# Kernel tuning notes

Measured on AMD Instinct MI355X. Metric: run time of the kernel, lower is better.

Reference implementation:

```python
import jax, jax.numpy as jnp
import numpy as np

ACTION_NS = [3, 3, 2, 4, 24]        # forward_back, left_right, jump, sneak_sprint, attack_...
RANGE_STARTS = [6, 8, 10, 11, 14]   # action_ranges starts (indices 0..5 are commit + camera ops)
N_ACTIONS = 37
LOGIT_DIM = 36
MIN_DELTA = 0.5 / 2**3
MAX_STEP = 20
MAX_CAMSTEP = 6
B, NUM_INPUT, HIDDEN = 32768, 1024, 2048
D_IN = NUM_INPUT + 4 + LOGIT_DIM


def setup_inputs():
    key = jax.random.key(0)
    ks = jax.random.split(key, 12)
    inp = {
        "fc_input": jax.random.normal(ks[0], (B, NUM_INPUT), jnp.float32),
        "camera": jax.random.normal(ks[1], (B, 2), jnp.float32),
        "rand_u": jax.random.uniform(ks[2], (B,), jnp.float32),
        "W1": (jax.random.normal(ks[3], (D_IN, HIDDEN), jnp.float32) / np.sqrt(D_IN)).astype(jnp.float32),
        "b1": jnp.zeros((HIDDEN,), jnp.float32),
        "W2": (jax.random.normal(ks[4], (HIDDEN, N_ACTIONS), jnp.float32) / np.sqrt(HIDDEN)).astype(jnp.float32),
        "b2": jnp.zeros((N_ACTIONS,), jnp.float32),
    }
    names = ["act_fb", "act_lr", "act_jp", "act_ss", "act_atk"]
    for i, (nm, n) in enumerate(zip(names, ACTION_NS)):
        inp[nm] = jax.random.randint(ks[5 + i], (B,), 0, n, jnp.int32)
    return inp


def _discretize_scan(camera, acts):
    # Faithful jax version of the 20-step no_grad target/input construction loop.
    nB = camera.shape[0]
    cam0, cam1 = camera[:, 0], camera[:, 1]

    def step(carry, _):
        ac, delta, rdac, dch, cam_steps, committed, norm = carry
        oh = [jax.nn.one_hot(r, n, dtype=jnp.float32) for r, n in zip(rdac, ACTION_NS)]
        inp_vec = jnp.concatenate([ac] + oh + [delta[:, None], dch.astype(jnp.float32)[:, None]], axis=1)  # [B,40]
        norm = norm + (~committed).astype(jnp.float32)
        commit = ((jnp.abs(cam0) < 1e-5) & (jnp.abs(cam1) < 1e-5)) | (cam_steps >= MAX_CAMSTEP)
        for r, a in zip(rdac, acts):
            commit = commit & (r == a)
        dac = jnp.zeros((nB,), jnp.int32)
        modified = commit
        new_rdac = []
        for r, a, rs in zip(rdac, acts, RANGE_STARTS):
            disc = (~modified) & (r != a)
            dac = jnp.where(disc & (a == 0), r - 1 + rs, jnp.where(disc, a - 1 + rs, dac))
            new_rdac.append(jnp.where(disc, a, r))
            modified = modified | disc
        d2 = delta * 2.0
        # NOTE: original torch code compares cam[:,1] against ac[:,0]; bug preserved.
        dmask = (~modified) & (~dch) & ((jnp.abs(cam0 - ac[:, 0]) > d2) | (jnp.abs(cam1 - ac[:, 0]) > d2))
        dac = jnp.where(dmask, 5, dac)
        delta = jnp.where(dmask, jnp.clip(d2, -0.5, 0.5), delta)
        modified = modified | dmask
        sx = jnp.where(cam0 < ac[:, 0], -1.0, 1.0)
        sy = jnp.where(cam1 < ac[:, 1], -1.0, 1.0)
        quad = jnp.where(sx < 0, jnp.where(sy < 0, 1, 3), jnp.where(sy < 0, 2, 4)).astype(jnp.int32)
        dac = jnp.where(~modified, quad, dac)
        move = jnp.stack([sx, sy], axis=1) * delta[:, None]
        ac = jnp.where((~modified)[:, None], ac + move, ac)
        delta = jnp.where(~modified, delta * 0.5, delta)
        dch = dch | (~modified)
        cam_steps = cam_steps + (~modified).astype(jnp.int32)
        committed = committed | commit
        return (ac, delta, tuple(new_rdac), dch, cam_steps, committed, norm), (inp_vec, dac)

    init = (jnp.zeros((nB, 2), jnp.float32),
            jnp.full((nB,), MIN_DELTA, jnp.float32),
            tuple(jnp.zeros((nB,), jnp.int32) for _ in ACTION_NS),
            jnp.zeros((nB,), bool),
            jnp.zeros((nB,), jnp.int32),
            jnp.zeros((nB,), bool),
            jnp.zeros((nB,), jnp.float32))
    carry, (all_inputs, all_dacs) = jax.lax.scan(step, init, None, length=MAX_STEP)
    return all_inputs, all_dacs, carry[-1]  # [T,B,40], [T,B], norm [B]


def reference(fc_input, camera, rand_u, W1, b1, W2, b2, act_fb, act_lr, act_jp, act_ss, act_atk):
    acts = (act_fb, act_lr, act_jp, act_ss, act_atk)
    all_inputs, all_dacs, norm = _discretize_scan(camera, acts)
    rand_sam = jnp.minimum((rand_u * norm).astype(jnp.int32), MAX_STEP - 1)  # sample an uncommitted step
    idx = jnp.arange(fc_input.shape[0])
    sel = jax.lax.stop_gradient(all_inputs[rand_sam, idx])  # [B,40]
    tgt = jax.lax.stop_gradient(all_dacs[rand_sam, idx])    # [B]
    x = jnp.concatenate([fc_input, sel], axis=1)
    h = x @ W1 + b1
    h = h * jax.nn.sigmoid(h)  # swish
    logits = h @ W2 + b2
    logp = jax.nn.log_softmax(logits, axis=-1)
    loss = -jnp.take_along_axis(logp, tgt[:, None], axis=1)[:, 0]  # per-sample CE (reduction='none')
    return loss
```

## Files before the change

kernel.cpp:

```cpp
#include <hip/hip_runtime.h>
#include <hip/hip_bf16.h>
#include <stdint.h>

#define B_ROWS 32768
#define NUM_IN 1024
#define D_PAD2 1088
#define HID    2048
#define NPAD   64

typedef __attribute__((ext_vector_type(8))) short bf16x8;
typedef __attribute__((ext_vector_type(4))) float f32x4;
typedef unsigned short ushort_t;

__device__ __forceinline__ unsigned short f2bf(float f){
  union { float f; uint32_t u; } x; x.f = f;
  uint32_t u = x.u;
  return (unsigned short)((u + 0x7FFFu + ((u >> 16) & 1u)) >> 16);
}

__device__ __forceinline__ void gload16(const void* g, void* l){
  __builtin_amdgcn_global_load_lds((const __attribute__((address_space(1))) void*)g,
                                   (__attribute__((address_space(3))) void*)l, 16, 0, 0);
}

__device__ __forceinline__ int disc_step(
    float cam0, float cam1, const int a[5],
    float& ac0, float& ac1, float& delta,
    int r[5], bool& dch, int& cam_steps, bool& committed, float& norm)
{
  const int RS[5] = {6, 8, 10, 11, 14};
  norm += committed ? 0.0f : 1.0f;
  bool commit = ((fabsf(cam0) < 1e-5f) && (fabsf(cam1) < 1e-5f)) || (cam_steps >= 6);
  #pragma unroll
  for (int i = 0; i < 5; ++i) commit = commit && (r[i] == a[i]);
  int dac = 0;
  bool modified = commit;
  #pragma unroll
  for (int i = 0; i < 5; ++i){
    bool disc = (!modified) && (r[i] != a[i]);
    if (disc){
      dac = (a[i] == 0) ? (r[i] - 1 + RS[i]) : (a[i] - 1 + RS[i]);
      r[i] = a[i];
      modified = true;
    }
  }
  float d2 = delta * 2.0f;
  bool dmask = (!modified) && (!dch) &&
               ((fabsf(cam0 - ac0) > d2) || (fabsf(cam1 - ac0) > d2));
  if (dmask){ dac = 5; delta = fminf(d2, 0.5f); modified = true; }
  if (!modified){
    float sx = (cam0 < ac0) ? -1.0f : 1.0f;
    float sy = (cam1 < ac1) ? -1.0f : 1.0f;
    dac = (sx < 0.0f) ? ((sy < 0.0f) ? 1 : 3) : ((sy < 0.0f) ? 2 : 4);
    ac0 += sx * delta; ac1 += sy * delta;
    delta *= 0.5f;
    dch = true;
    cam_steps += 1;
  }
  committed = committed || commit;
  return dac;
}

__global__ void k_prep(const float* __restrict__ fc, const float* __restrict__ W1,
                       const float* __restrict__ W2,
                       const float* __restrict__ camera, const float* __restrict__ rand_u,
                       const int* __restrict__ afb, const int* __restrict__ alr,
                       const int* __restrict__ ajp, const int* __restrict__ ass,
                       const int* __restrict__ aat,
                       unsigned short* __restrict__ xb, unsigned short* __restrict__ w1p,
                       unsigned short* __restrict__ w2t, int* __restrict__ tgt)
{
  __shared__ float lt[64][65];
  const int b = blockIdx.x;
  const int tid = threadIdx.x;
  if (b < 16384){
    int gid = b * 256 + tid;
    int row = gid >> 7;
    int c   = gid & 127;
    const float4* p = (const float4*)(fc + (size_t)row * NUM_IN + c * 8);
    float4 f0 = p[0], f1 = p[1];
    uint4 pk;
    pk.x = (uint32_t)f2bf(f0.x) | ((uint32_t)f2bf(f0.y) << 16);
    pk.y = (uint32_t)f2bf(f0.z) | ((uint32_t)f2bf(f0.w) << 16);
    pk.z = (uint32_t)f2bf(f1.x) | ((uint32_t)f2bf(f1.y) << 16);
    pk.w = (uint32_t)f2bf(f1.z) | ((uint32_t)f2bf(f1.w) << 16);
    *(uint4*)(xb + (size_t)row * D_PAD2 + c * 8) = pk;
    return;
  }
  if (b < 16928){
    const int bi = b - 16384;
    const int kt = bi % 17, nt = bi / 17;
    const int k0 = kt * 64, n0 = nt * 64;
    const int cgrp = nt >> 2, wn = nt & 3;
    const int c = tid & 63, rq = tid >> 6;
    #pragma unroll
    for (int rr = 0; rr < 16; ++rr){
      const int r = rr * 4 + rq;
      const int k = k0 + r;
      lt[r][c] = (k < 1064) ? W1[(size_t)k * HID + n0 + c] : 0.0f;
    }
    __syncthreads();
    #pragma unroll
    for (int s = 0; s < 2; ++s){
      const int idx = s * 256 + tid;
      const int ln = idx & 63, q = idx >> 6;
      const int lr2 = ln & 15, lg2 = ln >> 4;
      const int np = (q >> 2) * 32 + ((q >> 1) & 1) * 16 + lr2;
      const int kx = (q & 1) * 32 + lg2 * 8;
      uint4 pk;
      uint32_t w[4];
      #pragma unroll
      for (int e = 0; e < 4; ++e){
        unsigned short lo = f2bf(lt[kx + 2*e][np]);
        unsigned short hi = f2bf(lt[kx + 2*e + 1][np]);
        w[e] = (uint32_t)lo | ((uint32_t)hi << 16);
      }
      pk.x = w[0]; pk.y = w[1]; pk.z = w[2]; pk.w = w[3];
      *(uint4*)(w1p + (((size_t)cgrp*17 + kt) << 14) + (wn << 12) + q*512 + ln*8) = pk;
    }
    return;
  }
  if (b < 17440){
    int idx = (b - 16928) * 256 + tid;
    int n = idx >> 11;
    int k = idx & (HID - 1);
    float v = (n < 37) ? W2[(size_t)k * 37 + n] : 0.0f;
    w2t[idx] = f2bf(v);
    return;
  }
  int row = (b - 17440) * 256 + tid;
  float cam0 = camera[2*row], cam1 = camera[2*row + 1];
  int a[5] = { afb[row], alr[row], ajp[row], ass[row], aat[row] };

  float ac0 = 0.f, ac1 = 0.f, delta = 0.0625f, norm = 0.f;
  int r[5] = {0,0,0,0,0};
  bool dch = false, committed = false; int cam_steps = 0;
  for (int t = 0; t < 20; ++t)
    disc_step(cam0, cam1, a, ac0, ac1, delta, r, dch, cam_steps, committed, norm);

  int rs = (int)(rand_u[row] * norm);
  if (rs > 19) rs = 19;
  if (rs < 0) rs = 0;

  ac0 = 0.f; ac1 = 0.f; delta = 0.0625f; norm = 0.f;
  r[0]=r[1]=r[2]=r[3]=r[4]=0; dch = false; committed = false; cam_steps = 0;
  for (int t = 0; t < rs; ++t)
    disc_step(cam0, cam1, a, ac0, ac1, delta, r, dch, cam_steps, committed, norm);

  float vec[40];
  #pragma unroll
  for (int j = 0; j < 40; ++j) vec[j] = 0.0f;
  vec[0] = ac0; vec[1] = ac1;
  const int offs[5] = {2, 5, 8, 10, 14};
  #pragma unroll
  for (int i = 0; i < 5; ++i) vec[offs[i] + r[i]] = 1.0f;
  vec[38] = delta; vec[39] = dch ? 1.0f : 0.0f;

  int dac = disc_step(cam0, cam1, a, ac0, ac1, delta, r, dch, cam_steps, committed, norm);
  tgt[row] = dac;

  unsigned short* o = xb + (size_t)row * D_PAD2 + NUM_IN;
  #pragma unroll
  for (int j = 0; j < 40; ++j) o[j] = f2bf(vec[j]);
  #pragma unroll
  for (int j = 40; j < 64; ++j) o[j] = 0;
}


#define STAGE(REG, KT, HALF) do { \
    const ushort_t* s0_ = xb + (size_t)(brow + (HALF)*128 + srow) * D_PAD2 + ((KT) << 6) + scol; \
    gload16(s0_, lds + (REG) + (HALF)*8192 + t*8); \
    gload16(s0_ + (size_t)64 * D_PAD2, lds + (REG) + (HALF)*8192 + 4096 + t*8); \
  } while(0)

#define LDA_T(BO, MH) do { \
    _Pragma("unroll") for (int mi_ = 0; mi_ < 4; ++mi_) \
    _Pragma("unroll") for (int kk_ = 0; kk_ < 2; ++kk_) \
      aR[mi_][kk_] = *(const bf16x8*)(aBk[kk_] + (BO) + (((MH)*64 + mi_*16)*128)); \
  } while(0)

#define GLBH(BANK, KT, NH) do { \
    const ushort_t* bp_ = w1p + (((size_t)cgrp*17 + (KT)) << 14) + (wn << 12) + ((NH)*4)*512 + lane*8; \
    _Pragma("unroll") for (int ni_ = 0; ni_ < 2; ++ni_) \
    _Pragma("unroll") for (int kk_ = 0; kk_ < 2; ++kk_) \
      BANK[ni_][kk_] = *(const bf16x8*)(bp_ + (ni_*2 + kk_)*512); \
  } while(0)

#define MMA(MH, NH, BH) do { \
    __builtin_amdgcn_s_setprio(1); \
    _Pragma("unroll") for (int mi_ = 0; mi_ < 4; ++mi_) \
    _Pragma("unroll") for (int ni_ = 0; ni_ < 2; ++ni_) \
    _Pragma("unroll") for (int kk_ = 0; kk_ < 2; ++kk_) \
      acc[(MH)*4+mi_][(NH)*2+ni_] = __builtin_amdgcn_mfma_f32_16x16x32_bf16( \
          aR[mi_][kk_], BH[ni_][kk_], acc[(MH)*4+mi_][(NH)*2+ni_], 0, 0, 0); \
    __builtin_amdgcn_s_setprio(0); \
  } while(0)

#define BAR() __builtin_amdgcn_s_barrier()
#define WAIT_VM4() asm volatile("s_waitcnt vmcnt(4)" ::: "memory")
#define WAIT_VM0() asm volatile("s_waitcnt vmcnt(0)" ::: "memory")

__global__ __launch_bounds__(512, 2) void k_gemm1(const ushort_t* __restrict__ xb,
                                                  const ushort_t* __restrict__ w1p,
                                                  const ushort_t* __restrict__ w2t,
                                                  const float* __restrict__ b1,
                                                  float* __restrict__ pbuf)
{
  __shared__ ushort_t lds[65536];
  const int t = threadIdx.x;
  const int lane = t & 63;
  const int wid = t >> 6, wm = wid >> 2, wn = wid & 3;
  const int lr = lane & 15, lg = lane >> 4;

  const int bid = blockIdx.x;
  const int swz = (bid & 7) * 128 + (bid >> 3);
  const int brow = (swz >> 3) << 8;
  const int bcol = (swz & 7) << 8;
  const int cgrp = bcol >> 8;

  const int srow = t >> 3;
  const int scol = ((t & 7) ^ (srow & 7)) << 3;

  const int axor = lr & 7;
  const char* aBk[2];
  aBk[0] = (const char*)lds + (wm*128 + lr)*128 + (((0*4+lg)^axor) << 4);
  aBk[1] = (const char*)lds + (wm*128 + lr)*128 + (((1*4+lg)^axor) << 4);

  f32x4 acc[8][4] = {};
  bf16x8 aR[4][2];
  bf16x8 bH0[2][2], bH1[2][2];

  STAGE(0, 0, 0);  STAGE(0, 0, 1);
  GLBH(bH0, 0, 0); GLBH(bH1, 0, 1);
  STAGE(16384, 1, 0);  STAGE(16384, 1, 1);
  WAIT_VM4();
  BAR();

  #pragma unroll
  for (int tt = 0; tt < 17; ++tt){
    const int cbuf = (tt % 3) * 32768;
    const int sbo  = ((tt + 2) % 3) * 16384;
    const int st   = (tt + 2 <= 16) ? tt + 2 : 16;
    const int nk   = (tt + 1 <= 16) ? tt + 1 : 16;

    LDA_T(cbuf, 0);
    MMA(0, 0, bH0);
    MMA(0, 1, bH1);
    LDA_T(cbuf, 1);
    MMA(1, 0, bH0);
    GLBH(bH0, nk, 0);
    MMA(1, 1, bH1);
    GLBH(bH1, nk, 1);
    __builtin_amdgcn_sched_barrier(0);
    STAGE(sbo, st, 0);
    STAGE(sbo, st, 1);
    WAIT_VM4();
    BAR();
  }

  bf16x8 w2fA[4][4];
  #pragma unroll
  for (int ks = 0; ks < 4; ++ks)
    #pragma unroll
    for (int ni = 0; ni < 4; ++ni)
      w2fA[ks][ni] = *(const bf16x8*)(w2t + (size_t)(ni*16 + lr) * HID + bcol + ks*32 + lg*8);

  WAIT_VM0();
  BAR();

  float b1v[4];
  #pragma unroll
  for (int ni = 0; ni < 4; ++ni) b1v[ni] = b1[bcol + wn*64 + ni*16 + lr];

  #pragma unroll
  for (int mi = 0; mi < 8; ++mi){
    #pragma unroll
    for (int ni = 0; ni < 4; ++ni){
      const int col = wn*64 + ni*16 + lr;
      #pragma unroll
      for (int i2 = 0; i2 < 4; ++i2){
        const int row = wm*128 + mi*16 + lg*4 + i2;
        float v = acc[mi][ni][i2] + b1v[ni];
        float s = v / (1.0f + __expf(-v));
        const int chunk = (col >> 3) ^ (row & 7);
        lds[row*256 + chunk*8 + (col & 7)] = f2bf(s);
      }
    }
  }
  __syncthreads();

  bf16x8 w2fB[4][4];
  #pragma unroll
  for (int ks = 0; ks < 4; ++ks)
    #pragma unroll
    for (int ni = 0; ni < 4; ++ni)
      w2fB[ks][ni] = *(const bf16x8*)(w2t + (size_t)(ni*16 + lr) * HID + bcol + (ks+4)*32 + lg*8);

  const int rb = wid * 32;
  f32x4 acc2[2][4] = {};
  #pragma unroll
  for (int ks = 0; ks < 8; ++ks){
    bf16x8 a2[2];
    #pragma unroll
    for (int m = 0; m < 2; ++m){
      const int row = rb + m*16 + lr;
      a2[m] = *(const bf16x8*)(lds + row*256 + (((ks*4+lg) ^ (lr & 7)) << 3));
    }
    #pragma unroll
    for (int m = 0; m < 2; ++m)
      #pragma unroll
      for (int ni = 0; ni < 4; ++ni)
        acc2[m][ni] = __builtin_amdgcn_mfma_f32_16x16x32_bf16(
            a2[m], (ks < 4) ? w2fA[ks & 3][ni] : w2fB[ks & 3][ni], acc2[m][ni], 0, 0, 0);
  }

  const int cb = cgrp;
  #pragma unroll
  for (int m = 0; m < 2; ++m)
    #pragma unroll
    for (int ni = 0; ni < 4; ++ni)
      #pragma unroll
      for (int i2 = 0; i2 < 4; ++i2){
        const int r = brow + rb + m*16 + lg*4 + i2;
        pbuf[((size_t)cb << 21) + ((size_t)r << 6) + ni*16 + lr] = acc2[m][ni][i2];
      }
}

__global__ __launch_bounds__(256) void k_red(const float* __restrict__ pbuf,
                                             const float* __restrict__ b2,
                                             const int* __restrict__ tgt,
                                             float* __restrict__ loss)
{
  const int lane = threadIdx.x & 63, w = threadIdx.x >> 6;
  const int row0 = blockIdx.x * 128 + w * 32;
  const float bias = (lane < 37) ? b2[lane] : 0.0f;
  for (int i = 0; i < 32; ++i){
    const int r = row0 + i;
    float s = 0.0f;
    #pragma unroll
    for (int cb = 0; cb < 8; ++cb)
      s += pbuf[((size_t)cb << 21) + ((size_t)r << 6) + lane];
    float x = (lane < 37) ? (s + bias) : -1e30f;
    float m = x;
    #pragma unroll
    for (int off = 1; off < 64; off <<= 1) m = fmaxf(m, __shfl_xor(m, off, 64));
    float e = __expf(x - m);
    float se = e;
    #pragma unroll
    for (int off = 1; off < 64; off <<= 1) se += __shfl_xor(se, off, 64);
    const int tg = tgt[r];
    const float pick = __shfl(x, tg, 64);
    if (lane == 0) loss[r] = m + __logf(se) - pick;
  }
}

extern "C" void kernel_launch(void* const* d_in, const int* in_sizes, int n_in,
                              void* d_out, int out_size, void* d_ws, size_t ws_size,
                              hipStream_t stream)
{
  (void)in_sizes; (void)n_in; (void)out_size; (void)ws_size;
  const float* fc  = (const float*)d_in[0];
  const float* cam = (const float*)d_in[1];
  const float* ru  = (const float*)d_in[2];
  const float* W1  = (const float*)d_in[3];
  const float* b1  = (const float*)d_in[4];
  const float* W2  = (const float*)d_in[5];
  const float* b2  = (const float*)d_in[6];
  const int* afb = (const int*)d_in[7];
  const int* alr = (const int*)d_in[8];
  const int* ajp = (const int*)d_in[9];
  const int* ass = (const int*)d_in[10];
  const int* aat = (const int*)d_in[11];
  float* loss = (float*)d_out;

  char* ws = (char*)d_ws;
  unsigned short* xb  = (unsigned short*)(ws);
  unsigned short* w1p = (unsigned short*)(ws + 71303168);
  unsigned short* w2t = (unsigned short*)(ws + 75759616);
  int*            tgt = (int*)           (ws + 76021760);
  float*          pbuf= (float*)         (ws + 76152832);

  k_prep<<<17568, 256, 0, stream>>>(fc, W1, W2, cam, ru, afb, alr, ajp, ass, aat,
                                    xb, w1p, w2t, tgt);
  k_gemm1<<<(B_ROWS/256) * (HID/256), 512, 0, stream>>>(xb, w1p, w2t, b1, pbuf);
  k_red  <<<B_ROWS / 128, 256, 0, stream>>>(pbuf, b2, tgt, loss);
}
```

Measured before the change: 275.3 us.

## Fuse fp32-to-bf16 conversion of fc_input into GEMM1 A-tile staging

Drops the separate prep pass that converted fc_input to a padded bf16 buffer. GEMM1 now reads fp32 fc_input directly, converts it in registers and writes swizzled bf16 into LDS, taking only the 64-column discretization tail from a small side buffer. This avoids writing and re-reading a roughly 70 MB intermediate. In exchange, each GEMM block reads fp32 A data (twice the bytes), and each of the 8 column blocks rereads it. The async global-to-LDS loads become register round trips, which adds VGPR pressure and LDS-write stalls inside the MFMA loop.

```diff
diff --git a/kernel.cpp b/kernel.cpp
--- a/kernel.cpp
+++ b/kernel.cpp
@@ -4,7 +4,6 @@
 
 #define B_ROWS 32768
 #define NUM_IN 1024
-#define D_PAD2 1088
 #define HID    2048
 #define NPAD   64
 
@@ -16,11 +15,6 @@
   union { float f; uint32_t u; } x; x.f = f;
   uint32_t u = x.u;
   return (unsigned short)((u + 0x7FFFu + ((u >> 16) & 1u)) >> 16);
-}
-
-__device__ __forceinline__ void gload16(const void* g, void* l){
-  __builtin_amdgcn_global_load_lds((const __attribute__((address_space(1))) void*)g,
-                                   (__attribute__((address_space(3))) void*)l, 16, 0, 0);
 }
 
 __device__ __forceinline__ int disc_step(
@@ -61,35 +55,19 @@
   return dac;
 }
 
-__global__ void k_prep(const float* __restrict__ fc, const float* __restrict__ W1,
-                       const float* __restrict__ W2,
+__global__ void k_prep(const float* __restrict__ W1, const float* __restrict__ W2,
                        const float* __restrict__ camera, const float* __restrict__ rand_u,
                        const int* __restrict__ afb, const int* __restrict__ alr,
                        const int* __restrict__ ajp, const int* __restrict__ ass,
                        const int* __restrict__ aat,
-                       unsigned short* __restrict__ xb, unsigned short* __restrict__ w1p,
+                       unsigned short* __restrict__ xtail, unsigned short* __restrict__ w1p,
                        unsigned short* __restrict__ w2t, int* __restrict__ tgt)
 {
   __shared__ float lt[64][65];
   const int b = blockIdx.x;
   const int tid = threadIdx.x;
-  if (b < 16384){
-    int gid = b * 256 + tid;
-    int row = gid >> 7;
-    int c   = gid & 127;
-    const float4* p = (const float4*)(fc + (size_t)row * NUM_IN + c * 8);
-    float4 f0 = p[0], f1 = p[1];
-    uint4 pk;
-    pk.x = (uint32_t)f2bf(f0.x) | ((uint32_t)f2bf(f0.y) << 16);
-    pk.y = (uint32_t)f2bf(f0.z) | ((uint32_t)f2bf(f0.w) << 16);
-    pk.z = (uint32_t)f2bf(f1.x) | ((uint32_t)f2bf(f1.y) << 16);
-    pk.w = (uint32_t)f2bf(f1.z) | ((uint32_t)f2bf(f1.w) << 16);
-    *(uint4*)(xb + (size_t)row * D_PAD2 + c * 8) = pk;
-    return;
-  }
-  if (b < 16928){
-    const int bi = b - 16384;
-    const int kt = bi % 17, nt = bi / 17;
+  if (b < 544){
+    const int kt = b % 17, nt = b / 17;
     const int k0 = kt * 64, n0 = nt * 64;
     const int cgrp = nt >> 2, wn = nt & 3;
     const int c = tid & 63, rq = tid >> 6;
@@ -120,15 +98,15 @@
     }
     return;
   }
-  if (b < 17440){
-    int idx = (b - 16928) * 256 + tid;
+  if (b < 1056){
+    int idx = (b - 544) * 256 + tid;
     int n = idx >> 11;
     int k = idx & (HID - 1);
     float v = (n < 37) ? W2[(size_t)k * 37 + n] : 0.0f;
     w2t[idx] = f2bf(v);
     return;
   }
-  int row = (b - 17440) * 256 + tid;
+  int row = (b - 1056) * 256 + tid;
   float cam0 = camera[2*row], cam1 = camera[2*row + 1];
   int a[5] = { afb[row], alr[row], ajp[row], ass[row], aat[row] };
 
@@ -159,19 +137,13 @@
   int dac = disc_step(cam0, cam1, a, ac0, ac1, delta, r, dch, cam_steps, committed, norm);
   tgt[row] = dac;
 
-  unsigned short* o = xb + (size_t)row * D_PAD2 + NUM_IN;
+  unsigned short* o = xtail + (size_t)row * 64;
   #pragma unroll
   for (int j = 0; j < 40; ++j) o[j] = f2bf(vec[j]);
   #pragma unroll
   for (int j = 40; j < 64; ++j) o[j] = 0;
 }
 
-
-#define STAGE(REG, KT, HALF) do { \
-    const ushort_t* s0_ = xb + (size_t)(brow + (HALF)*128 + srow) * D_PAD2 + ((KT) << 6) + scol; \
-    gload16(s0_, lds + (REG) + (HALF)*8192 + t*8); \
-    gload16(s0_ + (size_t)64 * D_PAD2, lds + (REG) + (HALF)*8192 + 4096 + t*8); \
-  } while(0)
 
 #define LDA_T(BO, MH) do { \
     _Pragma("unroll") for (int mi_ = 0; mi_ < 4; ++mi_) \
@@ -196,11 +168,38 @@
     __builtin_amdgcn_s_setprio(0); \
   } while(0)
 
+#define LOADH(DST, KT, H) do { \
+    const float4* fp_ = (const float4*)(fc + (size_t)(brow + s_r) * NUM_IN + ((KT) << 6) + s_h*32 + (H)*16); \
+    _Pragma("unroll") for (int j_ = 0; j_ < 4; ++j_) DST[j_] = fp_[j_]; \
+  } while(0)
+
+#define WRITEH(SRC, SBO, H) do { \
+    _Pragma("unroll") for (int cc_ = 0; cc_ < 2; ++cc_){ \
+      float4 u_ = SRC[2*cc_], v_ = SRC[2*cc_ + 1]; \
+      uint4 pk_; \
+      pk_.x = (uint32_t)f2bf(u_.x) | ((uint32_t)f2bf(u_.y) << 16); \
+      pk_.y = (uint32_t)f2bf(u_.z) | ((uint32_t)f2bf(u_.w) << 16); \
+      pk_.z = (uint32_t)f2bf(v_.x) | ((uint32_t)f2bf(v_.y) << 16); \
+      pk_.w = (uint32_t)f2bf(v_.z) | ((uint32_t)f2bf(v_.w) << 16); \
+      const int ch_ = s_h*4 + (H)*2 + cc_; \
+      *(uint4*)(lds + (SBO) + s_r*64 + ((ch_ ^ (s_r & 7)) << 3)) = pk_; \
+    } \
+  } while(0)
+
+#define STAGE_TAIL(SBO) do { \
+    const uint4* tp_ = (const uint4*)(xtail + (size_t)(brow + s_r) * 64 + s_h*32); \
+    _Pragma("unroll") for (int c_ = 0; c_ < 4; ++c_){ \
+      uint4 pk_ = tp_[c_]; \
+      const int ch_ = s_h*4 + c_; \
+      *(uint4*)(lds + (SBO) + s_r*64 + ((ch_ ^ (s_r & 7)) << 3)) = pk_; \
+    } \
+  } while(0)
+
 #define BAR() __builtin_amdgcn_s_barrier()
-#define WAIT_VM4() asm volatile("s_waitcnt vmcnt(4)" ::: "memory")
-#define WAIT_VM0() asm volatile("s_waitcnt vmcnt(0)" ::: "memory")
-
-__global__ __launch_bounds__(512, 2) void k_gemm1(const ushort_t* __restrict__ xb,
+#define LGKM0() asm volatile("s_waitcnt lgkmcnt(0)" ::: "memory")
+
+__global__ __launch_bounds__(512, 2) void k_gemm1(const float* __restrict__ fc,
+                                                  const ushort_t* __restrict__ xtail,
                                                   const ushort_t* __restrict__ w1p,
                                                   const ushort_t* __restrict__ w2t,
                                                   const float* __restrict__ b1,
@@ -218,8 +217,8 @@
   const int bcol = (swz & 7) << 8;
   const int cgrp = bcol >> 8;
 
-  const int srow = t >> 3;
-  const int scol = ((t & 7) ^ (srow & 7)) << 3;
+  const int s_r = t >> 1;
+  const int s_h = t & 1;
 
   const int axor = lr & 7;
   const char* aBk[2];
@@ -230,10 +229,15 @@
   bf16x8 aR[4][2];
   bf16x8 bH0[2][2], bH1[2][2];
 
-  STAGE(0, 0, 0);  STAGE(0, 0, 1);
+  {
+    float4 fP[4];
+    LOADH(fP, 0, 0); WRITEH(fP, 0, 0);
+    LOADH(fP, 0, 1); WRITEH(fP, 0, 1);
+    LOADH(fP, 1, 0); WRITEH(fP, 16384, 0);
+    LOADH(fP, 1, 1); WRITEH(fP, 16384, 1);
+  }
   GLBH(bH0, 0, 0); GLBH(bH1, 0, 1);
-  STAGE(16384, 1, 0);  STAGE(16384, 1, 1);
-  WAIT_VM4();
+  LGKM0();
   BAR();
 
   #pragma unroll
@@ -243,18 +247,20 @@
     const int st   = (tt + 2 <= 16) ? tt + 2 : 16;
     const int nk   = (tt + 1 <= 16) ? tt + 1 : 16;
 
+    float4 fS0[4], fS1[4];
     LDA_T(cbuf, 0);
+    if (st < 16) LOADH(fS0, st, 0);
     MMA(0, 0, bH0);
     MMA(0, 1, bH1);
     LDA_T(cbuf, 1);
+    if (st < 16) LOADH(fS1, st, 1);
     MMA(1, 0, bH0);
     GLBH(bH0, nk, 0);
+    if (st < 16) WRITEH(fS0, sbo, 0);
     MMA(1, 1, bH1);
     GLBH(bH1, nk, 1);
-    __builtin_amdgcn_sched_barrier(0);
-    STAGE(sbo, st, 0);
-    STAGE(sbo, st, 1);
-    WAIT_VM4();
+    if (st < 16) { WRITEH(fS1, sbo, 1); } else { STAGE_TAIL(sbo); }
+    LGKM0();
     BAR();
   }
 
@@ -264,9 +270,6 @@
     #pragma unroll
     for (int ni = 0; ni < 4; ++ni)
       w2fA[ks][ni] = *(const bf16x8*)(w2t + (size_t)(ni*16 + lr) * HID + bcol + ks*32 + lg*8);
-
-  WAIT_VM0();
-  BAR();
 
   float b1v[4];
   #pragma unroll
@@ -374,14 +377,14 @@
   float* loss = (float*)d_out;
 
   char* ws = (char*)d_ws;
-  unsigned short* xb  = (unsigned short*)(ws);
-  unsigned short* w1p = (unsigned short*)(ws + 71303168);
-  unsigned short* w2t = (unsigned short*)(ws + 75759616);
-  int*            tgt = (int*)           (ws + 76021760);
-  float*          pbuf= (float*)         (ws + 76152832);
-
-  k_prep<<<17568, 256, 0, stream>>>(fc, W1, W2, cam, ru, afb, alr, ajp, ass, aat,
-                                    xb, w1p, w2t, tgt);
-  k_gemm1<<<(B_ROWS/256) * (HID/256), 512, 0, stream>>>(xb, w1p, w2t, b1, pbuf);
+  unsigned short* xtail = (unsigned short*)(ws);
+  unsigned short* w1p   = (unsigned short*)(ws + 4194304);
+  unsigned short* w2t   = (unsigned short*)(ws + 8650752);
+  int*            tgt   = (int*)           (ws + 8912896);
+  float*          pbuf  = (float*)         (ws + 9043968);
+
+  k_prep<<<1184, 256, 0, stream>>>(W1, W2, cam, ru, afb, alr, ajp, ass, aat,
+                                   xtail, w1p, w2t, tgt);
+  k_gemm1<<<(B_ROWS/256) * (HID/256), 512, 0, stream>>>(fc, xtail, w1p, w2t, b1, pbuf);
   k_red  <<<B_ROWS / 128, 256, 0, stream>>>(pbuf, b2, tgt, loss);
 }
```

Measured after the change: 310.1 us. +12.6%, slower.
